# Kernel tuning notes

Hardware: AMD Instinct MI355X
Metric: run time of the kernel (lower is better)

## Reference

```python
import jax, jax.numpy as jnp
import numpy as np

E = 40000   # num_entities
R = 474     # num_relations
D = 200     # Config.embedding_dim
L = 100     # n_num_lit
B = 32      # batch

def setup_inputs() -> dict:
    key = jax.random.key(0)
    ks = jax.random.split(key, 11)
    return {
        "e1": jax.random.randint(ks[0], (B, 1), 0, E),
        "rel": jax.random.randint(ks[1], (B, 1), 0, R),
        "emb_e": jax.random.normal(ks[2], (E, D), jnp.float32) * 0.1,           # emb_e.weight
        "emb_rel": jax.random.normal(ks[3], (R, D), jnp.float32) * 0.1,         # emb_rel.weight
        "num_lit": jax.random.normal(ks[4], (E, L), jnp.float32),               # numerical_literals (raw)
        "num_lit_norm": jax.random.uniform(ks[5], (E, L), jnp.float32),         # numerical_literals_normalized
        "W_lit": jax.random.normal(ks[6], (D, D + L), jnp.float32) / np.float32(np.sqrt(D + L)),  # emb_num_lit.weight
        "b_lit": jnp.zeros((D,), jnp.float32),                                  # emb_num_lit.bias
        "c": jax.random.normal(ks[7], (L,), jnp.float32),                       # RBF centers (fixed)
        "var": jax.random.uniform(ks[8], (L,), jnp.float32, minval=0.5, maxval=2.0),  # RBF variances (fixed)
        "nf_w": jax.random.normal(ks[9], (R, L), jnp.float32) * 0.1,            # nf_weights.weight
    }

def reference(e1, rel, emb_e, emb_rel, num_lit, num_lit_norm, W_lit, b_lit, c, var, nf_w):
    e1f = e1.reshape(-1)    # (B,)
    relf = rel.reshape(-1)  # (B,)
    # LiteralE gating via linear layer: emb_num_lit(cat([emb, lit]))
    e1_emb = jnp.concatenate([emb_e[e1f], num_lit_norm[e1f]], axis=1) @ W_lit.T + b_lit  # (B, D)
    e2_multi_emb = jnp.concatenate([emb_e, num_lit_norm], axis=1) @ W_lit.T + b_lit      # (E, D)
    rel_emb = emb_rel[relf]                                                              # (B, D)
    # dropout is identity at inference
    score_l = (e1_emb * rel_emb) @ e2_multi_emb.T  # (B, E)
    # KBLN numerical-literal score: broadcast diff + RBF + weighted reduction over literals
    n = num_lit[e1f][:, None, :] - num_lit[None, :, :]   # (B, E, L) -- large intermediate
    phi = jnp.exp(-jnp.square(n - c) / var)              # RBF, pointwise
    score_n = jnp.einsum('bel,bl->be', phi, nf_w[relf])  # bmm(phi, w_nf^T).squeeze()
    return jax.nn.sigmoid(score_l + score_n)             # (B, E)
```

## Files before the change

kernel.cpp:

```cpp
#include <hip/hip_runtime.h>
#include <math.h>

#define E_N 40000
#define D_N 200
#define L_N 100
#define K_N 300
#define B_N 32

typedef float  f32x4 __attribute__((ext_vector_type(4)));
typedef short  s16x8 __attribute__((ext_vector_type(8)));
typedef unsigned int u32x4 __attribute__((ext_vector_type(4)));

#define WS_SH 0
#define WS_W  3200
#define WS_NR 6400
#define WS_S0 6500
#define WS_PA 6532

#define SM_ML  6532
#define SM_TOT 9732
#define STAGE_N 2433

__device__ inline float fast_exp2(float x) {
#if __has_builtin(__builtin_amdgcn_exp2f)
    return __builtin_amdgcn_exp2f(x);
#else
    return exp2f(x);
#endif
}
__device__ inline float fast_rcp(float x) {
#if __has_builtin(__builtin_amdgcn_rcpf)
    return __builtin_amdgcn_rcpf(x);
#else
    return 1.0f / x;
#endif
}
__device__ inline ushort f2bf(float f) {
    uint u = __builtin_bit_cast(uint, f);
    u += 0x7fffu + ((u >> 16) & 1u);
    return (ushort)(u >> 16);
}
__device__ inline s16x8 pack_bf8(f32x4 lo, f32x4 hi) {
    uint r0, r1, r2, r3;
    asm("v_cvt_pk_bf16_f32 %0, %1, %2" : "=v"(r0) : "v"(lo[0]), "v"(lo[1]));
    asm("v_cvt_pk_bf16_f32 %0, %1, %2" : "=v"(r1) : "v"(lo[2]), "v"(lo[3]));
    asm("v_cvt_pk_bf16_f32 %0, %1, %2" : "=v"(r2) : "v"(hi[0]), "v"(hi[1]));
    asm("v_cvt_pk_bf16_f32 %0, %1, %2" : "=v"(r3) : "v"(hi[2]), "v"(hi[3]));
    u32x4 r = {r0, r1, r2, r3};
    return __builtin_bit_cast(s16x8, r);
}

__global__ __launch_bounds__(320) void prep_kernel(
    const int* __restrict__ e1, const int* __restrict__ rel,
    const float* __restrict__ emb_e, const float* __restrict__ emb_rel,
    const float* __restrict__ num_lit, const float* __restrict__ num_lit_norm,
    const float* __restrict__ W, const float* __restrict__ b_lit,
    const float* __restrict__ c, const float* __restrict__ var,
    const float* __restrict__ nf_w, float* __restrict__ ws)
{
    const int b = blockIdx.x;
    const int t = threadIdx.x;
    __shared__ float q[D_N];
    const int e1b = e1[b];
    const int rb  = rel[b];

    if (t < D_N) {
        const float* wr = W + t * K_N;
        const float* er = emb_e + (long)e1b * D_N;
        const float* nl = num_lit_norm + (long)e1b * L_N;
        float s0_ = b_lit[t], s1_ = 0.f, s2_ = 0.f, s3_ = 0.f;
        for (int k = 0; k < D_N; k += 4) {
            s0_ += er[k+0] * wr[k+0]; s1_ += er[k+1] * wr[k+1];
            s2_ += er[k+2] * wr[k+2]; s3_ += er[k+3] * wr[k+3];
        }
        for (int k = 0; k < L_N; k += 4) {
            s0_ += nl[k+0] * wr[D_N+k+0]; s1_ += nl[k+1] * wr[D_N+k+1];
            s2_ += nl[k+2] * wr[D_N+k+2]; s3_ += nl[k+3] * wr[D_N+k+3];
        }
        q[t] = ((s0_ + s1_) + (s2_ + s3_)) * emb_rel[rb * D_N + t];
    }
    __syncthreads();

    {
        float pk = 0.f;
        if (t < K_N) {
            float a0 = 0.f, a1 = 0.f, a2 = 0.f, a3 = 0.f;
            for (int d = 0; d < D_N; d += 4) {
                a0 += q[d+0] * W[(d+0) * K_N + t];
                a1 += q[d+1] * W[(d+1) * K_N + t];
                a2 += q[d+2] * W[(d+2) * K_N + t];
                a3 += q[d+3] * W[(d+3) * K_N + t];
            }
            pk = (a0 + a1) + (a2 + a3);
        }
        const int s  = t >> 5;
        const int g  = (t >> 3) & 3;
        const int j  = t & 7;
        const int mt = b >> 4;
        const int ln = (g << 4) | (b & 15);
        ushort* pa = (ushort*)(ws + WS_PA);
        pa[((mt * 10 + s) * 64 + ln) * 8 + j] = f2bf(pk);
    }

    if (t < L_N) {
        const float r = sqrtf(1.4426950408889634f / var[t]);
        ws[WS_SH + t * 32 + b] = r * (num_lit[(long)e1b * L_N + t] - c[t]);
        ws[WS_W  + t * 32 + b] = nf_w[rb * L_N + t];
        if (b == 0) ws[WS_NR + t] = -r;
    }
    if (t == 300) {
        float s = 0.f;
        for (int d = 0; d < D_N; ++d) s += q[d] * b_lit[d];
        ws[WS_S0 + b] = s;
    }
}

__global__ __launch_bounds__(256, 3) void score_kernel(
    const float* __restrict__ emb_e, const float* __restrict__ num_lit,
    const float* __restrict__ num_lit_norm, const float* __restrict__ ws,
    float* __restrict__ out)
{
    __shared__ float smem[SM_TOT];

    const int lane = threadIdx.x & 63;
    const int wv   = threadIdx.x >> 6;
    const int mt   = wv & 1;
    const int h    = wv >> 1;
    const int er   = lane & 15;
    const int g    = lane >> 4;
    const int ea   = blockIdx.x * 32 + er;
    const int eb   = ea + 16;
    const int b0   = mt * 16 + 4 * g;

    f32x4 acc_a = {0.f, 0.f, 0.f, 0.f};
    f32x4 acc_b = {0.f, 0.f, 0.f, 0.f};
    if (h == 0) {
        acc_a = *(const f32x4*)(ws + WS_S0 + b0);
        acc_b = acc_a;
    }

    s16x8 afr[5];
    {
        const s16x8* pAg = (const s16x8*)(ws + WS_PA);
#pragma unroll
        for (int i = 0; i < 5; ++i) afr[i] = pAg[(mt * 10 + h * 5 + i) * 64 + lane];
    }

    const float* embrA = emb_e        + (long)ea * D_N;
    const float* litnA = num_lit_norm + (long)ea * L_N;
    const float* embrB = emb_e        + (long)eb * D_N;
    const float* litnB = num_lit_norm + (long)eb * L_N;

    f32x4 loA[5], hiA[5], loB[5], hiB[5];
#pragma unroll
    for (int i = 0; i < 4; ++i) {
        const int k0 = 32 * (h * 5 + i) + 8 * g;
        const float* bpA = (k0 < 200) ? (embrA + k0) : (litnA + (k0 - 200));
        const float* bpB = (k0 < 200) ? (embrB + k0) : (litnB + (k0 - 200));
        loA[i] = *(const f32x4*)bpA;
        hiA[i] = *(const f32x4*)(bpA + 4);
        loB[i] = *(const f32x4*)bpB;
        hiB[i] = *(const f32x4*)(bpB + 4);
    }
    if (h == 0) {
        const int k0 = 128 + 8 * g;
        loA[4] = *(const f32x4*)(embrA + k0);
        hiA[4] = *(const f32x4*)(embrA + k0 + 4);
        loB[4] = *(const f32x4*)(embrB + k0);
        hiB[4] = *(const f32x4*)(embrB + k0 + 4);
    } else {
        f32x4 z = {0.f, 0.f, 0.f, 0.f};
        loA[4] = z; hiA[4] = z; loB[4] = z; hiB[4] = z;
        if (g == 0)      { loA[4] = *(const f32x4*)(litnA + 88); hiA[4] = *(const f32x4*)(litnA + 92);
                           loB[4] = *(const f32x4*)(litnB + 88); hiB[4] = *(const f32x4*)(litnB + 92); }
        else if (g == 1) { loA[4] = *(const f32x4*)(litnA + 96);
                           loB[4] = *(const f32x4*)(litnB + 96); }
    }

    {
        const f32x4* s4  = (const f32x4*)ws;
        const f32x4* ml4 = (const f32x4*)(num_lit + (long)blockIdx.x * 32 * L_N);
        f32x4* d4 = (f32x4*)smem;
        for (int i = threadIdx.x; i < STAGE_N; i += 256) {
            const f32x4* src = (i < 1633) ? (s4 + i) : (ml4 + (i - 1633));
            __builtin_amdgcn_global_load_lds((const __attribute__((address_space(1))) void*)src,
                                             (__attribute__((address_space(3))) void*)(d4 + i),
                                             16, 0, 0);
        }
    }

#pragma unroll
    for (int i = 0; i < 5; ++i) {
        acc_a = __builtin_amdgcn_mfma_f32_16x16x32_bf16(afr[i], pack_bf8(loA[i], hiA[i]), acc_a, 0, 0, 0);
        acc_b = __builtin_amdgcn_mfma_f32_16x16x32_bf16(afr[i], pack_bf8(loB[i], hiB[i]), acc_b, 0, 0, 0);
    }

    __syncthreads();

    const int lc0 = h ? 13 : 0;
    const int lcE = h ? 25 : 13;
    const float* mlA = smem + SM_ML + er * L_N;
    const float* mlB = mlA + 16 * L_N;
    for (int lc = lc0; lc < lcE; ++lc) {
        const f32x4 mva = *(const f32x4*)(mlA + lc * 4);
        const f32x4 mvb = *(const f32x4*)(mlB + lc * 4);
        const f32x4 nv  = *(const f32x4*)(smem + WS_NR + lc * 4);
#pragma unroll
        for (int ll = 0; ll < 4; ++ll) {
            const int l = lc * 4 + ll;
            const float rma = nv[ll] * mva[ll];
            const float rmb = nv[ll] * mvb[ll];
            f32x4 s4v = *(const f32x4*)(smem + WS_SH + l * 32 + b0);
            f32x4 w4v = *(const f32x4*)(smem + WS_W  + l * 32 + b0);
#pragma unroll
            for (int j = 0; j < 4; ++j) {
                const float ua = rma + s4v[j];
                const float ub = rmb + s4v[j];
                acc_a[j] = fmaf(fast_exp2(-(ua * ua)), w4v[j], acc_a[j]);
                acc_b[j] = fmaf(fast_exp2(-(ub * ub)), w4v[j], acc_b[j]);
            }
        }
    }

    float* cbuf = smem + SM_ML;
    __syncthreads();
    if (h) {
        *(f32x4*)(cbuf + ((0 * 2 + mt) * 64 + lane) * 4) = acc_a;
        *(f32x4*)(cbuf + ((1 * 2 + mt) * 64 + lane) * 4) = acc_b;
    }
    __syncthreads();
    if (!h) {
        const f32x4 oa = *(const f32x4*)(cbuf + ((0 * 2 + mt) * 64 + lane) * 4);
        const f32x4 ob = *(const f32x4*)(cbuf + ((1 * 2 + mt) * 64 + lane) * 4);
#pragma unroll
        for (int j = 0; j < 4; ++j) {
            const float va = acc_a[j] + oa[j];
            const float za = fast_exp2(va * -1.4426950408889634f);
            out[(long)(b0 + j) * E_N + ea] = fast_rcp(1.0f + za);
            const float vb = acc_b[j] + ob[j];
            const float zb = fast_exp2(vb * -1.4426950408889634f);
            out[(long)(b0 + j) * E_N + eb] = fast_rcp(1.0f + zb);
        }
    }
}

extern "C" void kernel_launch(void* const* d_in, const int* in_sizes, int n_in,
                              void* d_out, int out_size, void* d_ws, size_t ws_size,
                              hipStream_t stream) {
    const int*   e1       = (const int*)d_in[0];
    const int*   rel      = (const int*)d_in[1];
    const float* emb_e    = (const float*)d_in[2];
    const float* emb_rel  = (const float*)d_in[3];
    const float* num_lit  = (const float*)d_in[4];
    const float* num_lit_norm = (const float*)d_in[5];
    const float* W_lit    = (const float*)d_in[6];
    const float* b_lit    = (const float*)d_in[7];
    const float* c        = (const float*)d_in[8];
    const float* var      = (const float*)d_in[9];
    const float* nf_w     = (const float*)d_in[10];
    float* out = (float*)d_out;
    float* ws  = (float*)d_ws;

    hipLaunchKernelGGL(prep_kernel, dim3(B_N), dim3(320), 0, stream,
                       e1, rel, emb_e, emb_rel, num_lit, num_lit_norm,
                       W_lit, b_lit, c, var, nf_w, ws);
    hipLaunchKernelGGL(score_kernel, dim3(1250), dim3(256), 0, stream,
                       emb_e, num_lit, num_lit_norm, ws, out);
}
```

Before: 41.31 us.

## Split score kernel work across eight waves instead of four per block

```diff
diff --git a/kernel.cpp b/kernel.cpp
--- a/kernel.cpp
+++ b/kernel.cpp
@@ -115,7 +115,7 @@
     }
 }
 
-__global__ __launch_bounds__(256, 3) void score_kernel(
+__global__ __launch_bounds__(512, 2) void score_kernel(
     const float* __restrict__ emb_e, const float* __restrict__ num_lit,
     const float* __restrict__ num_lit_norm, const float* __restrict__ ws,
     float* __restrict__ out)
@@ -132,6 +132,9 @@
     const int eb   = ea + 16;
     const int b0   = mt * 16 + 4 * g;
 
+    const int st0 = (h < 2) ? 3 * h : 6 + 2 * (h - 2);
+    const int ns  = (h < 2) ? 3 : 2;
+
     f32x4 acc_a = {0.f, 0.f, 0.f, 0.f};
     f32x4 acc_b = {0.f, 0.f, 0.f, 0.f};
     if (h == 0) {
@@ -139,11 +142,12 @@
         acc_b = acc_a;
     }
 
-    s16x8 afr[5];
+    s16x8 afr[3];
     {
         const s16x8* pAg = (const s16x8*)(ws + WS_PA);
 #pragma unroll
-        for (int i = 0; i < 5; ++i) afr[i] = pAg[(mt * 10 + h * 5 + i) * 64 + lane];
+        for (int i = 0; i < 3; ++i)
+            if (i < ns) afr[i] = pAg[(mt * 10 + st0 + i) * 64 + lane];
     }
 
     const float* embrA = emb_e        + (long)ea * D_N;
@@ -151,37 +155,35 @@
     const float* embrB = emb_e        + (long)eb * D_N;
     const float* litnB = num_lit_norm + (long)eb * L_N;
 
-    f32x4 loA[5], hiA[5], loB[5], hiB[5];
-#pragma unroll
-    for (int i = 0; i < 4; ++i) {
-        const int k0 = 32 * (h * 5 + i) + 8 * g;
-        const float* bpA = (k0 < 200) ? (embrA + k0) : (litnA + (k0 - 200));
-        const float* bpB = (k0 < 200) ? (embrB + k0) : (litnB + (k0 - 200));
-        loA[i] = *(const f32x4*)bpA;
-        hiA[i] = *(const f32x4*)(bpA + 4);
-        loB[i] = *(const f32x4*)bpB;
-        hiB[i] = *(const f32x4*)(bpB + 4);
-    }
-    if (h == 0) {
-        const int k0 = 128 + 8 * g;
-        loA[4] = *(const f32x4*)(embrA + k0);
-        hiA[4] = *(const f32x4*)(embrA + k0 + 4);
-        loB[4] = *(const f32x4*)(embrB + k0);
-        hiB[4] = *(const f32x4*)(embrB + k0 + 4);
-    } else {
-        f32x4 z = {0.f, 0.f, 0.f, 0.f};
-        loA[4] = z; hiA[4] = z; loB[4] = z; hiB[4] = z;
-        if (g == 0)      { loA[4] = *(const f32x4*)(litnA + 88); hiA[4] = *(const f32x4*)(litnA + 92);
-                           loB[4] = *(const f32x4*)(litnB + 88); hiB[4] = *(const f32x4*)(litnB + 92); }
-        else if (g == 1) { loA[4] = *(const f32x4*)(litnA + 96);
-                           loB[4] = *(const f32x4*)(litnB + 96); }
+    f32x4 loA[3], hiA[3], loB[3], hiB[3];
+#pragma unroll
+    for (int i = 0; i < 3; ++i) {
+        if (i < ns) {
+            const int s = st0 + i;
+            if (s < 9) {
+                const int k0 = 32 * s + 8 * g;
+                const float* bpA = (k0 < 200) ? (embrA + k0) : (litnA + (k0 - 200));
+                const float* bpB = (k0 < 200) ? (embrB + k0) : (litnB + (k0 - 200));
+                loA[i] = *(const f32x4*)bpA;
+                hiA[i] = *(const f32x4*)(bpA + 4);
+                loB[i] = *(const f32x4*)bpB;
+                hiB[i] = *(const f32x4*)(bpB + 4);
+            } else {
+                f32x4 z = {0.f, 0.f, 0.f, 0.f};
+                loA[i] = z; hiA[i] = z; loB[i] = z; hiB[i] = z;
+                if (g == 0)      { loA[i] = *(const f32x4*)(litnA + 88); hiA[i] = *(const f32x4*)(litnA + 92);
+                                   loB[i] = *(const f32x4*)(litnB + 88); hiB[i] = *(const f32x4*)(litnB + 92); }
+                else if (g == 1) { loA[i] = *(const f32x4*)(litnA + 96);
+                                   loB[i] = *(const f32x4*)(litnB + 96); }
+            }
+        }
     }
 
     {
         const f32x4* s4  = (const f32x4*)ws;
         const f32x4* ml4 = (const f32x4*)(num_lit + (long)blockIdx.x * 32 * L_N);
         f32x4* d4 = (f32x4*)smem;
-        for (int i = threadIdx.x; i < STAGE_N; i += 256) {
+        for (int i = threadIdx.x; i < STAGE_N; i += 512) {
             const f32x4* src = (i < 1633) ? (s4 + i) : (ml4 + (i - 1633));
             __builtin_amdgcn_global_load_lds((const __attribute__((address_space(1))) void*)src,
                                              (__attribute__((address_space(3))) void*)(d4 + i),
@@ -190,15 +192,17 @@
     }
 
 #pragma unroll
-    for (int i = 0; i < 5; ++i) {
-        acc_a = __builtin_amdgcn_mfma_f32_16x16x32_bf16(afr[i], pack_bf8(loA[i], hiA[i]), acc_a, 0, 0, 0);
-        acc_b = __builtin_amdgcn_mfma_f32_16x16x32_bf16(afr[i], pack_bf8(loB[i], hiB[i]), acc_b, 0, 0, 0);
-    }
-
-    __syncthreads();
-
-    const int lc0 = h ? 13 : 0;
-    const int lcE = h ? 25 : 13;
+    for (int i = 0; i < 3; ++i) {
+        if (i < ns) {
+            acc_a = __builtin_amdgcn_mfma_f32_16x16x32_bf16(afr[i], pack_bf8(loA[i], hiA[i]), acc_a, 0, 0, 0);
+            acc_b = __builtin_amdgcn_mfma_f32_16x16x32_bf16(afr[i], pack_bf8(loB[i], hiB[i]), acc_b, 0, 0, 0);
+        }
+    }
+
+    __syncthreads();
+
+    const int lc0 = (h == 0) ? 0 : 7 + 6 * (h - 1);
+    const int lcE = (h == 0) ? 7 : lc0 + 6;
     const float* mlA = smem + SM_ML + er * L_N;
     const float* mlB = mlA + 16 * L_N;
     for (int lc = lc0; lc < lcE; ++lc) {
@@ -225,13 +229,20 @@
     float* cbuf = smem + SM_ML;
     __syncthreads();
     if (h) {
-        *(f32x4*)(cbuf + ((0 * 2 + mt) * 64 + lane) * 4) = acc_a;
-        *(f32x4*)(cbuf + ((1 * 2 + mt) * 64 + lane) * 4) = acc_b;
+        *(f32x4*)(cbuf + (((0 * 2 + mt) * 3 + (h - 1)) * 64 + lane) * 4) = acc_a;
+        *(f32x4*)(cbuf + (((1 * 2 + mt) * 3 + (h - 1)) * 64 + lane) * 4) = acc_b;
     }
     __syncthreads();
     if (!h) {
-        const f32x4 oa = *(const f32x4*)(cbuf + ((0 * 2 + mt) * 64 + lane) * 4);
-        const f32x4 ob = *(const f32x4*)(cbuf + ((1 * 2 + mt) * 64 + lane) * 4);
+        f32x4 oa = {0.f, 0.f, 0.f, 0.f};
+        f32x4 ob = {0.f, 0.f, 0.f, 0.f};
+#pragma unroll
+        for (int p = 0; p < 3; ++p) {
+            const f32x4 pa = *(const f32x4*)(cbuf + (((0 * 2 + mt) * 3 + p) * 64 + lane) * 4);
+            const f32x4 pb = *(const f32x4*)(cbuf + (((1 * 2 + mt) * 3 + p) * 64 + lane) * 4);
+#pragma unroll
+            for (int j = 0; j < 4; ++j) { oa[j] += pa[j]; ob[j] += pb[j]; }
+        }
 #pragma unroll
         for (int j = 0; j < 4; ++j) {
             const float va = acc_a[j] + oa[j];
@@ -264,6 +275,6 @@
     hipLaunchKernelGGL(prep_kernel, dim3(B_N), dim3(320), 0, stream,
                        e1, rel, emb_e, emb_rel, num_lit, num_lit_norm,
                        W_lit, b_lit, c, var, nf_w, ws);
-    hipLaunchKernelGGL(score_kernel, dim3(1250), dim3(256), 0, stream,
+    hipLaunchKernelGGL(score_kernel, dim3(1250), dim3(512), 0, stream,
                        emb_e, num_lit, num_lit_norm, ws, out);
 }
```

Result: no change. 41.89 us (+1.4%).
